# Kernel tuning notes

Hardware: AMD Instinct MI355X
Metric: run time of the kernel (lower is better)

## Reference

```python
import math
import jax, jax.numpy as jnp
import numpy as np

B, LA, LB, H = 32, 1024, 1024, 1024


def setup_inputs() -> dict:
    key = jax.random.key(0)
    k1, k2, k3, k4 = jax.random.split(key, 4)
    a = jax.random.normal(k1, (B, LA, H), dtype=jnp.float32)
    b = jax.random.normal(k2, (B, LB, H), dtype=jnp.float32)
    mask_a = jax.random.randint(k3, (B, LA, 1), 0, 2, dtype=jnp.int32)
    mask_b = jax.random.randint(k4, (B, LB, 1), 0, 2, dtype=jnp.int32)
    temperature = jnp.asarray(1.0 / math.sqrt(H), dtype=jnp.float32)
    return {"a": a, "b": b, "mask_a": mask_a, "mask_b": mask_b,
            "temperature": temperature}


def reference(a, b, mask_a, mask_b, temperature):
    # attn: [B, La, Lb] scaled cross-attention scores
    attn = jnp.einsum("bsh,bth->bst", a, b) * temperature
    # outer product of per-token validity -> pairwise valid mask [B, La, Lb]
    mask = jnp.einsum("bsi,bti->bst",
                      mask_a.astype(jnp.float32),
                      mask_b.astype(jnp.float32)).astype(bool)
    attn = jnp.where(mask, attn, jnp.float32(-10000.0))
    attn_a = jax.nn.softmax(attn, axis=1)  # normalize over La
    attn_b = jax.nn.softmax(attn, axis=2)  # normalize over Lb
    feature_b = jnp.einsum("bst,bsh->bth", attn_a, a)  # [B, Lb, H]
    feature_a = jnp.einsum("bst,bth->bsh", attn_b, b)  # [B, La, H]
    return feature_a, feature_b
```

## Files before the change

kernel.cpp:

```cpp
#include <hip/hip_runtime.h>

#define NB 32
#define L 1024
#define H 1024

typedef __attribute__((ext_vector_type(4))) float floatx4;
typedef __attribute__((ext_vector_type(8))) short shortx8;
typedef __attribute__((ext_vector_type(8))) unsigned short ushortx8;

__device__ __forceinline__ unsigned short f2bf(float f) {
    union { float f; unsigned int u; } v; v.f = f;
    unsigned int u = v.u;
    u += 0x7fffu + ((u >> 16) & 1u);
    return (unsigned short)(u >> 16);
}
__device__ __forceinline__ float bf2f(unsigned short h) {
    union { unsigned int u; float f; } v; v.u = ((unsigned int)h) << 16;
    return v.f;
}

__device__ __forceinline__ void gload_lds16(const void* g, void* l) {
    __builtin_amdgcn_global_load_lds(
        (const __attribute__((address_space(1))) unsigned int*)g,
        (__attribute__((address_space(3))) unsigned int*)l, 16, 0, 0);
}

__global__ void detect_kernel(const unsigned short* a, int* flag) {
    int tid = threadIdx.x;
    unsigned short u = a[tid];
    int e = (u >> 7) & 0xff;
    int ok = (u == 0) || (e >= 116 && e <= 136);
    unsigned long long ball = __ballot(ok != 0);
    if (tid == 0) flag[0] = (__popcll(ball) >= 56) ? 1 : 0;
}

__device__ __forceinline__ void store_out(void* out, size_t eidx, float v, int isbf) {
    if (isbf) ((unsigned short*)out)[eidx] = f2bf(v);
    else      ((float*)out)[eidx] = v;
}

__global__ __launch_bounds__(256) void convT_kernel(
    const void* A, const void* Bm, const int* flag,
    unsigned short* a_c, unsigned short* b_c,
    unsigned short* aT, unsigned short* bT,
    float* mean_a, float* mean_b, int b0) {
    __shared__ __align__(16) unsigned short T[64][80];
    int z = blockIdx.z;
    int which = z & 1, bi_l = z >> 1, bi = b0 + bi_l;
    int s0 = blockIdx.y * 64, h0 = blockIdx.x * 64;
    const void* src = which ? Bm : A;
    unsigned short* xc = which ? b_c : a_c;
    unsigned short* xT = which ? bT : aT;
    float* msum = which ? mean_b : mean_a;
    int isbf = flag[0];
    int tid = threadIdx.x;

    int r = tid >> 2, c0 = (tid & 3) * 16;
    size_t gin = (size_t)bi * L * H + (size_t)(s0 + r) * H + h0 + c0;
    unsigned short v[16];
    if (isbf) {
        const unsigned short* p = (const unsigned short*)src + gin;
        *(ushortx8*)&v[0] = *(const ushortx8*)p;
        *(ushortx8*)&v[8] = *(const ushortx8*)(p + 8);
    } else {
        const float* p = (const float*)src + gin;
#pragma unroll
        for (int u = 0; u < 16; u += 4) {
            float4 f = *(const float4*)(p + u);
            v[u] = f2bf(f.x); v[u + 1] = f2bf(f.y);
            v[u + 2] = f2bf(f.z); v[u + 3] = f2bf(f.w);
        }
    }
    *(ushortx8*)&T[r][c0] = *(const ushortx8*)&v[0];
    *(ushortx8*)&T[r][c0 + 8] = *(const ushortx8*)&v[8];
    size_t gco = (size_t)bi_l * L * H + (size_t)(s0 + r) * H + h0 + c0;
    *(ushortx8*)&xc[gco] = *(const ushortx8*)&v[0];
    *(ushortx8*)&xc[gco + 8] = *(const ushortx8*)&v[8];
    __syncthreads();

    int hr = tid >> 2, sc0 = (tid & 3) * 16;
    unsigned short tv2[16];
    float ms = 0.f;
#pragma unroll
    for (int u = 0; u < 16; ++u) {
        unsigned short q = T[sc0 + u][hr];
        tv2[u] = q;
        ms += bf2f(q);
    }
    size_t gto = (size_t)bi_l * (size_t)H * L + (size_t)(h0 + hr) * L + s0 + sc0;
    *(ushortx8*)&xT[gto] = *(const ushortx8*)&tv2[0];
    *(ushortx8*)&xT[gto + 8] = *(const ushortx8*)&tv2[8];
    ms += __shfl_xor(ms, 1);
    ms += __shfl_xor(ms, 2);
    if ((tid & 3) == 0) atomicAdd(&msum[bi * H + h0 + hr], ms);
}

__global__ __launch_bounds__(256) void wtrans_kernel(const unsigned short* w,
                                                     unsigned short* wT) {
    __shared__ __align__(16) unsigned short T[64][80];
    int bi_l = blockIdx.z;
    int s0 = blockIdx.y * 64, t0 = blockIdx.x * 64;
    int tid = threadIdx.x;
    int r = tid >> 2, c0 = (tid & 3) * 16;
    size_t gin = (size_t)bi_l * L * L + (size_t)(s0 + r) * L + t0 + c0;
    *(ushortx8*)&T[r][c0] = *(const ushortx8*)&w[gin];
    *(ushortx8*)&T[r][c0 + 8] = *(const ushortx8*)&w[gin + 8];
    __syncthreads();
    int tr = tid >> 2, sc0 = (tid & 3) * 16;
    unsigned short o[16];
#pragma unroll
    for (int u = 0; u < 16; ++u) o[u] = T[sc0 + u][tr];
    size_t gout = (size_t)bi_l * L * L + (size_t)(t0 + tr) * L + s0 + sc0;
    *(ushortx8*)&wT[gout] = *(const ushortx8*)&o[0];
    *(ushortx8*)&wT[gout + 8] = *(const ushortx8*)&o[8];
}

__device__ __forceinline__ void gemm_kk(
    const unsigned short* Arow, const unsigned short* Brow,
    int lda, int ldb, int K,
    unsigned short* AsBase, unsigned short* BsBase,
    int tid, floatx4 (&acc)[4][4]) {
    int lane = tid & 63;
    int wid = tid >> 6;
    int wm = wid >> 1, wn = wid & 1;
    int lane15 = lane & 15, quad = lane >> 4;

    for (int k0 = 0; k0 < K; k0 += 32) {
#pragma unroll
        for (int it = 0; it < 4; ++it) {
            int idx = (it & 1) * 256 + tid;
            int rr = idx >> 2, cc = (idx & 3) * 8;
            const unsigned short* src = (it < 2)
                ? (Arow + (size_t)rr * lda + k0 + cc)
                : (Brow + (size_t)rr * ldb + k0 + cc);
            unsigned short* dst = ((it < 2) ? AsBase : BsBase) + idx * 8;
            gload_lds16(src, dst);
        }
        __syncthreads();
        shortx8 af[4], bfr[4];
#pragma unroll
        for (int i = 0; i < 4; ++i)
            af[i] = *(const shortx8*)(AsBase + (wm * 64 + i * 16 + lane15) * 32 + quad * 8);
#pragma unroll
        for (int j = 0; j < 4; ++j)
            bfr[j] = *(const shortx8*)(BsBase + (wn * 64 + j * 16 + lane15) * 32 + quad * 8);
#pragma unroll
        for (int i = 0; i < 4; ++i)
#pragma unroll
            for (int j = 0; j < 4; ++j)
                acc[i][j] = __builtin_amdgcn_mfma_f32_16x16x32_bf16(af[i], bfr[j], acc[i][j], 0, 0, 0);
        __syncthreads();
    }
}

__global__ __launch_bounds__(256) void score_kernel(
    const unsigned short* a_c, const unsigned short* b_c,
    const int* mask_a, const int* mask_b, const void* temp, const int* flag,
    unsigned short* w, float* row_l, float* col_l, int b0) {
    __shared__ __align__(16) unsigned short As[128 * 32];
    __shared__ __align__(16) unsigned short Bs[128 * 32];
    int bi_l = blockIdx.z, bi = b0 + bi_l;
    int s0 = blockIdx.y * 128, t0 = blockIdx.x * 128;
    int tid = threadIdx.x;

    floatx4 acc[4][4];
#pragma unroll
    for (int i = 0; i < 4; ++i)
#pragma unroll
        for (int j = 0; j < 4; ++j)
#pragma unroll
            for (int rr = 0; rr < 4; ++rr) acc[i][j][rr] = 0.f;

    gemm_kk(a_c + (size_t)bi_l * L * H + (size_t)s0 * H,
            b_c + (size_t)bi_l * L * H + (size_t)t0 * H,
            H, H, H, As, Bs, tid, acc);

    int isbf = flag[0];
    float tv = isbf ? bf2f(((const unsigned short*)temp)[0]) : ((const float*)temp)[0];
    int lane = tid & 63, wid = tid >> 6;
    int wm = wid >> 1, wn = wid & 1;
    int lane15 = lane & 15, quad = lane >> 4;

    int mb[4];
#pragma unroll
    for (int j = 0; j < 4; ++j)
        mb[j] = mask_b[bi * L + t0 + wn * 64 + j * 16 + lane15];
    size_t wbase = (size_t)bi_l * L * L;
    float colp[4] = {0.f, 0.f, 0.f, 0.f};
#pragma unroll
    for (int i = 0; i < 4; ++i) {
#pragma unroll
        for (int r = 0; r < 4; ++r) {
            int s = s0 + wm * 64 + i * 16 + quad * 4 + r;
            int ma = mask_a[bi * L + s];
            float rp = 0.f;
#pragma unroll
            for (int j = 0; j < 4; ++j) {
                int t = t0 + wn * 64 + j * 16 + lane15;
                float wv = (ma && mb[j]) ? __expf(acc[i][j][r] * tv) : 0.f;
                unsigned short wq = f2bf(wv);
                w[wbase + (size_t)s * L + t] = wq;
                float wf = bf2f(wq);
                rp += wf;
                colp[j] += wf;
            }
            rp += __shfl_xor(rp, 1);
            rp += __shfl_xor(rp, 2);
            rp += __shfl_xor(rp, 4);
            rp += __shfl_xor(rp, 8);
            if (lane15 == 0) atomicAdd(&row_l[bi * L + s], rp);
        }
    }
#pragma unroll
    for (int j = 0; j < 4; ++j) {
        float cp = colp[j];
        cp += __shfl_xor(cp, 16);
        cp += __shfl_xor(cp, 32);
        if (quad == 0) {
            int t = t0 + wn * 64 + j * 16 + lane15;
            atomicAdd(&col_l[bi * L + t], cp);
        }
    }
}

__global__ __launch_bounds__(256) void feat_a_kernel(
    const unsigned short* w, const unsigned short* bT, const int* mask_a,
    const int* flag, const float* row_l, const float* mean_b, void* out, int b0) {
    __shared__ __align__(16) unsigned short As[128 * 32];
    __shared__ __align__(16) unsigned short Bs[128 * 32];
    int bi_l = blockIdx.z, bi = b0 + bi_l;
    int s0 = blockIdx.y * 128, h0 = blockIdx.x * 128;
    int tid = threadIdx.x;

    floatx4 acc[4][4];
#pragma unroll
    for (int i = 0; i < 4; ++i)
#pragma unroll
        for (int j = 0; j < 4; ++j)
#pragma unroll
            for (int rr = 0; rr < 4; ++rr) acc[i][j][rr] = 0.f;

    gemm_kk(w + (size_t)bi_l * L * L + (size_t)s0 * L,
            bT + (size_t)bi_l * (size_t)H * L + (size_t)h0 * L,
            L, L, L, As, Bs, tid, acc);

    int isbf = flag[0];
    int lane = tid & 63, wid = tid >> 6;
    int wm = wid >> 1, wn = wid & 1;
    int lane15 = lane & 15, quad = lane >> 4;
    const float invL = 1.f / (float)L;
#pragma unroll
    for (int i = 0; i < 4; ++i) {
#pragma unroll
        for (int r = 0; r < 4; ++r) {
            int s = s0 + wm * 64 + i * 16 + quad * 4 + r;
            int ma = mask_a[bi * L + s];
            float scale = ma ? (1.f / row_l[bi * L + s]) : 0.f;
#pragma unroll
            for (int j = 0; j < 4; ++j) {
                int h = h0 + wn * 64 + j * 16 + lane15;
                float v = ma ? acc[i][j][r] * scale : mean_b[bi * H + h] * invL;
                store_out(out, (size_t)bi * L * H + (size_t)s * H + h, v, isbf);
            }
        }
    }
}

__global__ __launch_bounds__(256) void feat_b_kernel(
    const unsigned short* wT, const unsigned short* aT, const int* mask_b,
    const int* flag, const float* col_l, const float* mean_a, void* out, int b0) {
    __shared__ __align__(16) unsigned short As[128 * 32];
    __shared__ __align__(16) unsigned short Bs[128 * 32];
    int bi_l = blockIdx.z, bi = b0 + bi_l;
    int t0 = blockIdx.y * 128, h0 = blockIdx.x * 128;
    int tid = threadIdx.x;

    floatx4 acc[4][4];
#pragma unroll
    for (int i = 0; i < 4; ++i)
#pragma unroll
        for (int j = 0; j < 4; ++j)
#pragma unroll
            for (int rr = 0; rr < 4; ++rr) acc[i][j][rr] = 0.f;

    gemm_kk(wT + (size_t)bi_l * L * L + (size_t)t0 * L,
            aT + (size_t)bi_l * (size_t)H * L + (size_t)h0 * L,
            L, L, L, As, Bs, tid, acc);

    int isbf = flag[0];
    int lane = tid & 63, wid = tid >> 6;
    int wm = wid >> 1, wn = wid & 1;
    int lane15 = lane & 15, quad = lane >> 4;
    const float invL = 1.f / (float)L;
    const size_t FEAT_B_OFF = (size_t)NB * L * H;
#pragma unroll
    for (int i = 0; i < 4; ++i) {
#pragma unroll
        for (int r = 0; r < 4; ++r) {
            int t = t0 + wm * 64 + i * 16 + quad * 4 + r;
            int mbv = mask_b[bi * L + t];
            float scale = mbv ? (1.f / col_l[bi * L + t]) : 0.f;
#pragma unroll
            for (int j = 0; j < 4; ++j) {
                int h = h0 + wn * 64 + j * 16 + lane15;
                float v = mbv ? acc[i][j][r] * scale : mean_a[bi * H + h] * invL;
                store_out(out, FEAT_B_OFF + (size_t)bi * L * H + (size_t)t * H + h, v, isbf);
            }
        }
    }
}

extern "C" void kernel_launch(void* const* d_in, const int* in_sizes, int n_in,
                              void* d_out, int out_size, void* d_ws, size_t ws_size,
                              hipStream_t stream) {
    const void* a = d_in[0];
    const void* b = d_in[1];
    const int* mask_a = (const int*)d_in[2];
    const int* mask_b = (const int*)d_in[3];
    const void* temp = d_in[4];

    char* wsp = (char*)d_ws;
    float* row_l  = (float*)wsp;
    float* col_l  = row_l + (size_t)NB * L;
    float* mean_a = col_l + (size_t)NB * L;
    float* mean_b = mean_a + (size_t)NB * H;
    int*   flag   = (int*)(mean_b + (size_t)NB * H);
    const size_t stats_bytes = ((size_t)NB * L * 2 + (size_t)NB * H * 2) * 4 + 256;

    const size_t per_batch = 6 * (size_t)L * H * 2;
    size_t wavail = (ws_size > stats_bytes) ? ws_size - stats_bytes : 0;
    int chunk = (int)(wavail / per_batch);
    if (chunk < 1) chunk = 1;
    if (chunk > NB) chunk = NB;

    unsigned short* a_c  = (unsigned short*)(wsp + stats_bytes);
    unsigned short* b_c  = a_c + (size_t)chunk * L * H;
    unsigned short* aT   = b_c + (size_t)chunk * L * H;
    unsigned short* bT   = aT  + (size_t)chunk * L * H;
    unsigned short* wbuf = bT  + (size_t)chunk * L * H;
    unsigned short* wT   = wbuf + (size_t)chunk * L * L;

    hipMemsetAsync(d_ws, 0, stats_bytes, stream);
    detect_kernel<<<1, 64, 0, stream>>>((const unsigned short*)a, flag);

    for (int b0 = 0; b0 < NB; b0 += chunk) {
        int nb = (NB - b0 < chunk) ? (NB - b0) : chunk;
        convT_kernel<<<dim3(16, 16, nb * 2), 256, 0, stream>>>(
            a, b, flag, a_c, b_c, aT, bT, mean_a, mean_b, b0);
        score_kernel<<<dim3(8, 8, nb), 256, 0, stream>>>(
            a_c, b_c, mask_a, mask_b, temp, flag, wbuf, row_l, col_l, b0);
        wtrans_kernel<<<dim3(16, 16, nb), 256, 0, stream>>>(wbuf, wT);
        feat_a_kernel<<<dim3(8, 8, nb), 256, 0, stream>>>(
            wbuf, bT, mask_a, flag, row_l, mean_b, d_out, b0);
        feat_b_kernel<<<dim3(8, 8, nb), 256, 0, stream>>>(
            wT, aT, mask_b, flag, col_l, mean_a, d_out, b0);
    }
}
```

Baseline: 917.4 us.

## Fuse score transpose into score kernel, swizzle tiles across XCDs, skip bf16 copy

Removes the separate wtrans kernel: the score kernel now also writes the transposed exp-weight matrix through an LDS slab, so the weight matrix is no longer re-read from global memory to transpose it. All GEMM kernels switch to a 1D grid with a swizzle that maps consecutive block IDs onto tiles in an XCD-aware order, aiming for better L2 locality. When inputs are already bf16, the score GEMM reads the raw inputs directly and convT skips writing the contiguous copy. The cost is extra LDS traffic and syncs in the score epilogue, plus recomputing exp for the transposed write.

```diff
diff --git a/kernel.cpp b/kernel.cpp
--- a/kernel.cpp
+++ b/kernel.cpp
@@ -23,6 +23,15 @@
     __builtin_amdgcn_global_load_lds(
         (const __attribute__((address_space(1))) unsigned int*)g,
         (__attribute__((address_space(3))) unsigned int*)l, 16, 0, 0);
+}
+
+__device__ __forceinline__ void swz_tile(int nb, int& bi_l, int& tx, int& ty) {
+    int fid = blockIdx.x;
+    int wid = (fid & 7) * (nb * 8) + (fid >> 3);
+    bi_l = wid >> 6;
+    int t = wid & 63;
+    tx = t & 7;
+    ty = t >> 3;
 }
 
 __global__ void detect_kernel(const unsigned short* a, int* flag) {
@@ -73,9 +82,11 @@
     }
     *(ushortx8*)&T[r][c0] = *(const ushortx8*)&v[0];
     *(ushortx8*)&T[r][c0 + 8] = *(const ushortx8*)&v[8];
-    size_t gco = (size_t)bi_l * L * H + (size_t)(s0 + r) * H + h0 + c0;
-    *(ushortx8*)&xc[gco] = *(const ushortx8*)&v[0];
-    *(ushortx8*)&xc[gco + 8] = *(const ushortx8*)&v[8];
+    if (!isbf) {
+        size_t gco = (size_t)bi_l * L * H + (size_t)(s0 + r) * H + h0 + c0;
+        *(ushortx8*)&xc[gco] = *(const ushortx8*)&v[0];
+        *(ushortx8*)&xc[gco + 8] = *(const ushortx8*)&v[8];
+    }
     __syncthreads();
 
     int hr = tid >> 2, sc0 = (tid & 3) * 16;
@@ -93,26 +104,6 @@
     ms += __shfl_xor(ms, 1);
     ms += __shfl_xor(ms, 2);
     if ((tid & 3) == 0) atomicAdd(&msum[bi * H + h0 + hr], ms);
-}
-
-__global__ __launch_bounds__(256) void wtrans_kernel(const unsigned short* w,
-                                                     unsigned short* wT) {
-    __shared__ __align__(16) unsigned short T[64][80];
-    int bi_l = blockIdx.z;
-    int s0 = blockIdx.y * 64, t0 = blockIdx.x * 64;
-    int tid = threadIdx.x;
-    int r = tid >> 2, c0 = (tid & 3) * 16;
-    size_t gin = (size_t)bi_l * L * L + (size_t)(s0 + r) * L + t0 + c0;
-    *(ushortx8*)&T[r][c0] = *(const ushortx8*)&w[gin];
-    *(ushortx8*)&T[r][c0 + 8] = *(const ushortx8*)&w[gin + 8];
-    __syncthreads();
-    int tr = tid >> 2, sc0 = (tid & 3) * 16;
-    unsigned short o[16];
-#pragma unroll
-    for (int u = 0; u < 16; ++u) o[u] = T[sc0 + u][tr];
-    size_t gout = (size_t)bi_l * L * L + (size_t)(t0 + tr) * L + s0 + sc0;
-    *(ushortx8*)&wT[gout] = *(const ushortx8*)&o[0];
-    *(ushortx8*)&wT[gout + 8] = *(const ushortx8*)&o[8];
 }
 
 __device__ __forceinline__ void gemm_kk(
@@ -154,14 +145,20 @@
 }
 
 __global__ __launch_bounds__(256) void score_kernel(
+    const void* Araw, const void* Braw,
     const unsigned short* a_c, const unsigned short* b_c,
     const int* mask_a, const int* mask_b, const void* temp, const int* flag,
-    unsigned short* w, float* row_l, float* col_l, int b0) {
-    __shared__ __align__(16) unsigned short As[128 * 32];
-    __shared__ __align__(16) unsigned short Bs[128 * 32];
-    int bi_l = blockIdx.z, bi = b0 + bi_l;
-    int s0 = blockIdx.y * 128, t0 = blockIdx.x * 128;
-    int tid = threadIdx.x;
+    unsigned short* w, unsigned short* wT,
+    float* row_l, float* col_l, int b0, int nb) {
+    __shared__ __align__(16) unsigned short lds_all[8192];
+    unsigned short* As = lds_all;
+    unsigned short* Bs = lds_all + 4096;
+    int bi_l, tx, ty;
+    swz_tile(nb, bi_l, tx, ty);
+    int bi = b0 + bi_l;
+    int s0 = ty * 128, t0 = tx * 128;
+    int tid = threadIdx.x;
+    int isbf = flag[0];
 
     floatx4 acc[4][4];
 #pragma unroll
@@ -171,11 +168,14 @@
 #pragma unroll
             for (int rr = 0; rr < 4; ++rr) acc[i][j][rr] = 0.f;
 
-    gemm_kk(a_c + (size_t)bi_l * L * H + (size_t)s0 * H,
-            b_c + (size_t)bi_l * L * H + (size_t)t0 * H,
-            H, H, H, As, Bs, tid, acc);
-
-    int isbf = flag[0];
+    const unsigned short* Arow = isbf
+        ? (const unsigned short*)Araw + (size_t)bi * L * H + (size_t)s0 * H
+        : a_c + (size_t)bi_l * L * H + (size_t)s0 * H;
+    const unsigned short* Brow = isbf
+        ? (const unsigned short*)Braw + (size_t)bi * L * H + (size_t)t0 * H
+        : b_c + (size_t)bi_l * L * H + (size_t)t0 * H;
+    gemm_kk(Arow, Brow, H, H, H, As, Bs, tid, acc);
+
     float tv = isbf ? bf2f(((const unsigned short*)temp)[0]) : ((const float*)temp)[0];
     int lane = tid & 63, wid = tid >> 6;
     int wm = wid >> 1, wn = wid & 1;
@@ -221,15 +221,43 @@
             atomicAdd(&col_l[bi * L + t], cp);
         }
     }
+
+    unsigned short* slab = lds_all;
+    int c = wn * 16 + lane15;
+    for (int j = 0; j < 4; ++j) {
+        __syncthreads();
+#pragma unroll
+        for (int i = 0; i < 4; ++i) {
+#pragma unroll
+            for (int r = 0; r < 4; ++r) {
+                int sl = wm * 64 + i * 16 + quad * 4 + r;
+                int ma = mask_a[bi * L + s0 + sl];
+                float wv = (ma && mb[j]) ? __expf(acc[i][j][r] * tv) : 0.f;
+                slab[sl * 34 + c] = f2bf(wv);
+            }
+        }
+        __syncthreads();
+        int cc = tid >> 3, sch = (tid & 7) * 16;
+        __align__(16) unsigned short o[16];
+#pragma unroll
+        for (int u = 0; u < 16; ++u) o[u] = slab[(sch + u) * 34 + cc];
+        int t = t0 + (cc >> 4) * 64 + j * 16 + (cc & 15);
+        size_t go = (size_t)bi_l * L * L + (size_t)t * L + s0 + sch;
+        *(ushortx8*)&wT[go] = *(const ushortx8*)&o[0];
+        *(ushortx8*)&wT[go + 8] = *(const ushortx8*)&o[8];
+    }
 }
 
 __global__ __launch_bounds__(256) void feat_a_kernel(
     const unsigned short* w, const unsigned short* bT, const int* mask_a,
-    const int* flag, const float* row_l, const float* mean_b, void* out, int b0) {
+    const int* flag, const float* row_l, const float* mean_b, void* out,
+    int b0, int nb) {
     __shared__ __align__(16) unsigned short As[128 * 32];
     __shared__ __align__(16) unsigned short Bs[128 * 32];
-    int bi_l = blockIdx.z, bi = b0 + bi_l;
-    int s0 = blockIdx.y * 128, h0 = blockIdx.x * 128;
+    int bi_l, tx, ty;
+    swz_tile(nb, bi_l, tx, ty);
+    int bi = b0 + bi_l;
+    int s0 = ty * 128, h0 = tx * 128;
     int tid = threadIdx.x;
 
     floatx4 acc[4][4];
@@ -268,11 +296,14 @@
 
 __global__ __launch_bounds__(256) void feat_b_kernel(
     const unsigned short* wT, const unsigned short* aT, const int* mask_b,
-    const int* flag, const float* col_l, const float* mean_a, void* out, int b0) {
+    const int* flag, const float* col_l, const float* mean_a, void* out,
+    int b0, int nb) {
     __shared__ __align__(16) unsigned short As[128 * 32];
     __shared__ __align__(16) unsigned short Bs[128 * 32];
-    int bi_l = blockIdx.z, bi = b0 + bi_l;
-    int t0 = blockIdx.y * 128, h0 = blockIdx.x * 128;
+    int bi_l, tx, ty;
+    swz_tile(nb, bi_l, tx, ty);
+    int bi = b0 + bi_l;
+    int t0 = ty * 128, h0 = tx * 128;
     int tid = threadIdx.x;
 
     floatx4 acc[4][4];
@@ -347,12 +378,12 @@
         int nb = (NB - b0 < chunk) ? (NB - b0) : chunk;
         convT_kernel<<<dim3(16, 16, nb * 2), 256, 0, stream>>>(
             a, b, flag, a_c, b_c, aT, bT, mean_a, mean_b, b0);
-        score_kernel<<<dim3(8, 8, nb), 256, 0, stream>>>(
-            a_c, b_c, mask_a, mask_b, temp, flag, wbuf, row_l, col_l, b0);
-        wtrans_kernel<<<dim3(16, 16, nb), 256, 0, stream>>>(wbuf, wT);
-        feat_a_kernel<<<dim3(8, 8, nb), 256, 0, stream>>>(
-            wbuf, bT, mask_a, flag, row_l, mean_b, d_out, b0);
-        feat_b_kernel<<<dim3(8, 8, nb), 256, 0, stream>>>(
-            wT, aT, mask_b, flag, col_l, mean_a, d_out, b0);
-    }
-}
+        score_kernel<<<dim3(nb * 64), 256, 0, stream>>>(
+            a, b, a_c, b_c, mask_a, mask_b, temp, flag, wbuf, wT,
+            row_l, col_l, b0, nb);
+        feat_a_kernel<<<dim3(nb * 64), 256, 0, stream>>>(
+            wbuf, bT, mask_a, flag, row_l, mean_b, d_out, b0, nb);
+        feat_b_kernel<<<dim3(nb * 64), 256, 0, stream>>>(
+            wT, aT, mask_b, flag, col_l, mean_a, d_out, b0, nb);
+    }
+}
```

Result: no change. 909.9 us (-0.8%).
